# Optimization experiments

Hardware: AMD Instinct MI355X
Metric: run time of the kernel (lower is better)

## Reference

```python
import jax, jax.numpy as jnp
import numpy as np

B, S, D = 1, 2048, 1024          # batch, seq, hidden_size
E, K, F = 8, 2, 1408             # n_routed_experts, top_k, moe_intermediate_size
NS = 2                           # n_shared_experts
SCALE = 2.5                      # routed_scaling_factor (norm_topk_prob=True)


def setup_inputs() -> dict:
    key = jax.random.key(0)
    ks = jax.random.split(key, 8)
    s = 0.02
    return {
        "hidden_states": jax.random.normal(ks[0], (B, S, D), jnp.float32),
        "gate_w": jax.random.normal(ks[1], (E, D), jnp.float32) * s,
        "w_gate": jax.random.normal(ks[2], (E, D, F), jnp.float32) * s,
        "w_up": jax.random.normal(ks[3], (E, D, F), jnp.float32) * s,
        "w_down": jax.random.normal(ks[4], (E, F, D), jnp.float32) * s,
        "sw_gate": jax.random.normal(ks[5], (D, F * NS), jnp.float32) * s,
        "sw_up": jax.random.normal(ks[6], (D, F * NS), jnp.float32) * s,
        "sw_down": jax.random.normal(ks[7], (F * NS, D), jnp.float32) * s,
    }


def _swiglu_mlp(x, wg, wu, wd):
    # down( silu(gate(x)) * up(x) )
    return (jax.nn.silu(x @ wg) * (x @ wu)) @ wd


def reference(hidden_states, gate_w, w_gate, w_up, w_down, sw_gate, sw_up, sw_down):
    identity = hidden_states
    x = hidden_states.reshape(-1, hidden_states.shape[-1])  # [T, D]
    T = x.shape[0]

    # --- MoEGate (softmax scoring, greedy top-k, normalized + scaled) ---
    logits = x.astype(jnp.float32) @ gate_w.astype(jnp.float32).T  # [T, E]
    scores = jax.nn.softmax(logits, axis=-1)
    topk_w, topk_i = jax.lax.top_k(scores, K)                      # [T, K]
    topk_w = topk_w / (topk_w.sum(-1, keepdims=True) + 1e-20) * SCALE

    # Dense combine weights [T, E]: topk weight where routed, 0 elsewhere.
    combine = jnp.zeros((T, E), jnp.float32).at[
        jnp.arange(T)[:, None], topk_i
    ].set(topk_w)

    # --- Routed experts as grouped GEMMs (same math as sort/dispatch loop) ---
    g = jax.nn.silu(jnp.einsum('td,edf->etf', x, w_gate)) \
        * jnp.einsum('td,edf->etf', x, w_up)                       # [E, T, F]
    expert_out = jnp.einsum('etf,efd->etd', g, w_down)             # [E, T, D]
    y = jnp.einsum('te,etd->td', combine, expert_out).astype(x.dtype)
    y = y.reshape(identity.shape)

    # --- Shared expert ---
    return y + _swiglu_mlp(identity, sw_gate, sw_up, sw_down)
```

## Files before the change

kernel.cpp:

```cpp
#include <hip/hip_runtime.h>
#include <hip/hip_bf16.h>
#include <stdint.h>

#define TT 2048
#define DD 1024
#define NE 8
#define FR 1408
#define FS 2816
#define RSCALE 2.5f
#define NSLOT (TT * 2)
#define TSH 4096

typedef __attribute__((ext_vector_type(8))) short bf16x8;
typedef __attribute__((ext_vector_type(4))) float f32x4;

__device__ __forceinline__ short f2bf(float f) {
  uint32_t u = __builtin_bit_cast(uint32_t, f);
  u = (u + 0x7fffu + ((u >> 16) & 1u)) >> 16;
  return (short)(uint16_t)u;
}

__global__ void cast_kernel(const float* __restrict__ in, short* __restrict__ out, int n) {
  int i = (blockIdx.x * blockDim.x + threadIdx.x) * 4;
  if (i >= n) return;
  float4 v = *(const float4*)(in + i);
  short4 o;
  o.x = f2bf(v.x); o.y = f2bf(v.y); o.z = f2bf(v.z); o.w = f2bf(v.w);
  *(short4*)(out + i) = o;
}

__global__ void __launch_bounds__(256) tcastV(const float* __restrict__ in0,
                                              const float* __restrict__ in1,
                                              short* __restrict__ out0, short* __restrict__ out1,
                                              int K, int N, int64_t zin, int64_t zout, int nz) {
  int z = blockIdx.z;
  const float* in;
  short* out;
  if (z < nz) { in = in0 + (int64_t)z * zin; out = out0 + (int64_t)z * zout; }
  else        { int zz = z - nz; in = in1 + (int64_t)zz * zin; out = out1 + (int64_t)zz * zout; }
  __shared__ float tile[32][33];
  const int k0 = blockIdx.y * 32, n0 = blockIdx.x * 32;
  const int tid = threadIdx.x;
  const int lr = tid >> 5, lc = tid & 31;
#pragma unroll
  for (int i = 0; i < 4; ++i)
    tile[lr + i * 8][lc] = in[(int64_t)(k0 + lr + i * 8) * N + n0 + lc];
  __syncthreads();
  const int nl = tid >> 3, kq = (tid & 7) * 4;
  short4 o;
  o.x = f2bf(tile[kq + 0][nl]); o.y = f2bf(tile[kq + 1][nl]);
  o.z = f2bf(tile[kq + 2][nl]); o.w = f2bf(tile[kq + 3][nl]);
  *(short4*)&out[(int64_t)(n0 + nl) * K + k0 + kq] = o;
}

__global__ void gate_kernel(const float* __restrict__ x, const float* __restrict__ gw,
                            int* __restrict__ te, float* __restrict__ tw) {
  int t = blockIdx.x;
  int lane = threadIdx.x;
  const float* xr = x + (size_t)t * DD + lane * 16;
  float4 xv[4];
#pragma unroll
  for (int i = 0; i < 4; ++i) xv[i] = *(const float4*)(xr + i * 4);
  float p[NE];
#pragma unroll
  for (int e = 0; e < NE; ++e) {
    const float* gr = gw + (size_t)e * DD + lane * 16;
    float s = 0.f;
#pragma unroll
    for (int i = 0; i < 4; ++i) {
      float4 g = *(const float4*)(gr + i * 4);
      s += xv[i].x * g.x + xv[i].y * g.y + xv[i].z * g.z + xv[i].w * g.w;
    }
    p[e] = s;
  }
#pragma unroll
  for (int off = 32; off >= 1; off >>= 1) {
#pragma unroll
    for (int e = 0; e < NE; ++e) p[e] += __shfl_xor(p[e], off);
  }
  float mx = p[0];
#pragma unroll
  for (int e = 1; e < NE; ++e) mx = fmaxf(mx, p[e]);
  float s = 0.f, sc[NE];
#pragma unroll
  for (int e = 0; e < NE; ++e) { sc[e] = expf(p[e] - mx); s += sc[e]; }
  float inv = 1.f / s;
#pragma unroll
  for (int e = 0; e < NE; ++e) sc[e] *= inv;
  int e1 = 0;
#pragma unroll
  for (int e = 1; e < NE; ++e) if (sc[e] > sc[e1]) e1 = e;
  int e2 = (e1 == 0) ? 1 : 0;
#pragma unroll
  for (int e = 0; e < NE; ++e) if (e != e1 && sc[e] > sc[e2]) e2 = e;
  float w1 = sc[e1], w2 = sc[e2];
  float k = RSCALE / (w1 + w2 + 1e-20f);
  if (lane == 0) {
    te[t * 2] = e1;     tw[t * 2] = w1 * k;
    te[t * 2 + 1] = e2; tw[t * 2 + 1] = w2 * k;
  }
}

__global__ void __launch_bounds__(1024) scatter_kernel(const int* __restrict__ te,
                                                       const float* __restrict__ tw,
                                                       int* __restrict__ cnt, int* __restrict__ off,
                                                       int* __restrict__ eidx, float* __restrict__ wslot) {
  __shared__ int lcnt[NE], loff[NE], lrun[NE];
  const int tid = threadIdx.x;
  if (tid < NE) lcnt[tid] = 0;
  __syncthreads();
  for (int s = tid; s < NSLOT; s += 1024) atomicAdd(&lcnt[te[s]], 1);
  __syncthreads();
  if (tid == 0) {
    int acc = 0;
    for (int e = 0; e < NE; ++e) { loff[e] = acc; lrun[e] = acc; acc += lcnt[e]; }
  }
  __syncthreads();
  for (int s = tid; s < NSLOT; s += 1024) {
    int e = te[s];
    int p = atomicAdd(&lrun[e], 1);
    eidx[p] = s >> 1;
    wslot[p] = tw[s];
  }
  if (tid < NE) { cnt[tid] = lcnt[tid]; off[tid] = loff[tid]; }
}

__device__ __forceinline__ void stage32(const short* __restrict__ g, int64_t ld,
                                        short* l, int wave, int lane) {
#pragma unroll
  for (int i = 0; i < 2; ++i) {
    int c = i * 256 + wave * 64 + lane;
    __builtin_amdgcn_global_load_lds(
        (const __attribute__((address_space(1))) void*)(g + (int64_t)(c >> 2) * ld + (c & 3) * 8),
        (__attribute__((address_space(3))) void*)(l + (i * 256 + wave * 64) * 8),
        16, 0, 0);
  }
}

template <int MODE>
__global__ void __launch_bounds__(256) moe_gemm(
    const short* __restrict__ Ab, int lda,
    const short* __restrict__ B0b, const short* __restrict__ B1b, int ldb,
    int K,
    short* __restrict__ Hb, int ldh,
    float* __restrict__ Ob) {
  const int brow = blockIdx.y * 128;
  const int bcol = blockIdx.x * 128;

  __shared__ __align__(16) short lA[2 * TSH];
  __shared__ __align__(16) short lB0[2 * TSH];
  __shared__ __align__(16) short lB1[(MODE == 0) ? 2 * TSH : 8];

  const int tid = threadIdx.x;
  const int lane = tid & 63;
  const int wave = tid >> 6;
  const int wr = wave >> 1, wc = wave & 1;

  f32x4 acc0[4][4];
  f32x4 acc1[(MODE == 0) ? 4 : 1][(MODE == 0) ? 4 : 1];
#pragma unroll
  for (int m = 0; m < 4; ++m)
#pragma unroll
    for (int n = 0; n < 4; ++n) {
      acc0[m][n] = (f32x4){0.f, 0.f, 0.f, 0.f};
      if constexpr (MODE == 0) acc1[m][n] = (f32x4){0.f, 0.f, 0.f, 0.f};
    }

  const short* Abase = Ab + (int64_t)brow * lda;
  const short* B0base = B0b + (int64_t)bcol * ldb;
  const short* B1base = (MODE == 0) ? (B1b + (int64_t)bcol * ldb) : nullptr;

  auto STAGE = [&](int buf, int k0) {
    stage32(Abase + k0, lda, lA + buf * TSH, wave, lane);
    stage32(B0base + k0, ldb, lB0 + buf * TSH, wave, lane);
    if constexpr (MODE == 0) stage32(B1base + k0, ldb, lB1 + buf * TSH, wave, lane);
  };

  STAGE(0, 0);
  __syncthreads();
  int cur = 0;
  for (int k0 = 0; k0 < K; k0 += 32) {
    if (k0 + 32 < K) STAGE(cur ^ 1, k0 + 32);
    const short* A_ = lA + cur * TSH;
    const short* B0_ = lB0 + cur * TSH;
    const short* B1_ = lB1 + cur * TSH;
#pragma unroll
    for (int m = 0; m < 4; ++m) {
      bf16x8 af = *(const bf16x8*)&A_[(wr * 64 + m * 16 + (lane & 15)) * 32 + (lane >> 4) * 8];
#pragma unroll
      for (int n = 0; n < 4; ++n) {
        bf16x8 b0 = *(const bf16x8*)&B0_[(wc * 64 + n * 16 + (lane & 15)) * 32 + (lane >> 4) * 8];
        acc0[m][n] = __builtin_amdgcn_mfma_f32_16x16x32_bf16(af, b0, acc0[m][n], 0, 0, 0);
        if constexpr (MODE == 0) {
          bf16x8 b1 = *(const bf16x8*)&B1_[(wc * 64 + n * 16 + (lane & 15)) * 32 + (lane >> 4) * 8];
          acc1[m][n] = __builtin_amdgcn_mfma_f32_16x16x32_bf16(af, b1, acc1[m][n], 0, 0, 0);
        }
      }
    }
    __syncthreads();
    cur ^= 1;
  }

#pragma unroll
  for (int m = 0; m < 4; ++m)
#pragma unroll
    for (int n = 0; n < 4; ++n)
#pragma unroll
      for (int r = 0; r < 4; ++r) {
        int row = brow + wr * 64 + m * 16 + (lane >> 4) * 4 + r;
        int col = bcol + wc * 64 + n * 16 + (lane & 15);
        float g = acc0[m][n][r];
        if constexpr (MODE == 0) {
          float u = acc1[m][n][r];
          Hb[(int64_t)row * ldh + col] = f2bf(g / (1.f + __expf(-g)) * u);
        } else {
          Ob[(int64_t)row * DD + col] = g;
        }
      }
}

__global__ void __launch_bounds__(256) gu_sparse(
    const short* __restrict__ Xb,
    const short* __restrict__ wgT, const short* __restrict__ wuT,
    short* __restrict__ Hr,
    const int* __restrict__ cnt, const int* __restrict__ off,
    const int* __restrict__ eidx) {
  const int z = blockIdx.z;
  const int c = cnt[z];
  const int m0 = blockIdx.y * 128;
  if (m0 >= c) return;
  const int base = off[z];
  const int bcol = blockIdx.x * 128;

  __shared__ __align__(16) short lA[2 * TSH];
  __shared__ __align__(16) short lB0[2 * TSH];
  __shared__ __align__(16) short lB1[2 * TSH];

  const int tid = threadIdx.x;
  const int lane = tid & 63;
  const int wave = tid >> 6;
  const int wr = wave >> 1, wc = wave & 1;

  const short* aptr[2];
#pragma unroll
  for (int i = 0; i < 2; ++i) {
    int cl = i * 256 + wave * 64 + lane;
    int r = cl >> 2;
    int sv = m0 + r; if (sv >= c) sv = c - 1;
    aptr[i] = Xb + (int64_t)eidx[base + sv] * DD + (cl & 3) * 8;
  }

  f32x4 acc0[4][4], acc1[4][4];
#pragma unroll
  for (int m = 0; m < 4; ++m)
#pragma unroll
    for (int n = 0; n < 4; ++n) {
      acc0[m][n] = (f32x4){0.f, 0.f, 0.f, 0.f};
      acc1[m][n] = (f32x4){0.f, 0.f, 0.f, 0.f};
    }

  const short* B0base = wgT + (int64_t)z * FR * DD + (int64_t)bcol * DD;
  const short* B1base = wuT + (int64_t)z * FR * DD + (int64_t)bcol * DD;

  auto STAGE = [&](int buf, int k0) {
#pragma unroll
    for (int i = 0; i < 2; ++i)
      __builtin_amdgcn_global_load_lds(
          (const __attribute__((address_space(1))) void*)(aptr[i] + k0),
          (__attribute__((address_space(3))) void*)(lA + buf * TSH + (i * 256 + wave * 64) * 8),
          16, 0, 0);
    stage32(B0base + k0, DD, lB0 + buf * TSH, wave, lane);
    stage32(B1base + k0, DD, lB1 + buf * TSH, wave, lane);
  };

  STAGE(0, 0);
  __syncthreads();
  int cur = 0;
  for (int k0 = 0; k0 < DD; k0 += 32) {
    if (k0 + 32 < DD) STAGE(cur ^ 1, k0 + 32);
    const short* A_ = lA + cur * TSH;
    const short* B0_ = lB0 + cur * TSH;
    const short* B1_ = lB1 + cur * TSH;
#pragma unroll
    for (int m = 0; m < 4; ++m) {
      bf16x8 af = *(const bf16x8*)&A_[(wr * 64 + m * 16 + (lane & 15)) * 32 + (lane >> 4) * 8];
#pragma unroll
      for (int n = 0; n < 4; ++n) {
        bf16x8 b0 = *(const bf16x8*)&B0_[(wc * 64 + n * 16 + (lane & 15)) * 32 + (lane >> 4) * 8];
        acc0[m][n] = __builtin_amdgcn_mfma_f32_16x16x32_bf16(af, b0, acc0[m][n], 0, 0, 0);
        bf16x8 b1 = *(const bf16x8*)&B1_[(wc * 64 + n * 16 + (lane & 15)) * 32 + (lane >> 4) * 8];
        acc1[m][n] = __builtin_amdgcn_mfma_f32_16x16x32_bf16(af, b1, acc1[m][n], 0, 0, 0);
      }
    }
    __syncthreads();
    cur ^= 1;
  }

#pragma unroll
  for (int m = 0; m < 4; ++m)
#pragma unroll
    for (int n = 0; n < 4; ++n)
#pragma unroll
      for (int r = 0; r < 4; ++r) {
        int rl = wr * 64 + m * 16 + (lane >> 4) * 4 + r;
        int sv = m0 + rl;
        if (sv < c) {
          int col = bcol + wc * 64 + n * 16 + (lane & 15);
          float g = acc0[m][n][r], u = acc1[m][n][r];
          Hr[(int64_t)(base + sv) * FR + col] = f2bf(g / (1.f + __expf(-g)) * u);
        }
      }
}

__global__ void __launch_bounds__(256) down_sparse(
    const short* __restrict__ Hr,
    const short* __restrict__ wdT,
    float* __restrict__ out,
    const int* __restrict__ cnt, const int* __restrict__ off,
    const int* __restrict__ eidx, const float* __restrict__ wslot) {
  const int z = blockIdx.z;
  const int c = cnt[z];
  const int m0 = blockIdx.y * 128;
  if (m0 >= c) return;
  const int base = off[z];
  const int bcol = blockIdx.x * 128;

  __shared__ __align__(16) short lA[2 * TSH];
  __shared__ __align__(16) short lB0[2 * TSH];
  __shared__ int lTok[128];
  __shared__ float lW[128];

  const int tid = threadIdx.x;
  const int lane = tid & 63;
  const int wave = tid >> 6;
  const int wr = wave >> 1, wc = wave & 1;

  if (tid < 128) {
    int sv = m0 + tid;
    if (sv < c) { lTok[tid] = eidx[base + sv]; lW[tid] = wslot[base + sv]; }
    else lW[tid] = 0.f;
  }

  f32x4 acc0[4][4];
#pragma unroll
  for (int m = 0; m < 4; ++m)
#pragma unroll
    for (int n = 0; n < 4; ++n) acc0[m][n] = (f32x4){0.f, 0.f, 0.f, 0.f};

  const short* B0base = wdT + (int64_t)z * DD * FR + (int64_t)bcol * FR;

  auto STAGE = [&](int buf, int k0) {
#pragma unroll
    for (int i = 0; i < 2; ++i) {
      int cl = i * 256 + wave * 64 + lane;
      int r = cl >> 2;
      int sv = m0 + r; if (sv >= c) sv = c - 1;
      __builtin_amdgcn_global_load_lds(
          (const __attribute__((address_space(1))) void*)(Hr + (int64_t)(base + sv) * FR + k0 + (cl & 3) * 8),
          (__attribute__((address_space(3))) void*)(lA + buf * TSH + (i * 256 + wave * 64) * 8),
          16, 0, 0);
    }
    stage32(B0base + k0, FR, lB0 + buf * TSH, wave, lane);
  };

  STAGE(0, 0);
  __syncthreads();
  int cur = 0;
  for (int k0 = 0; k0 < FR; k0 += 32) {
    if (k0 + 32 < FR) STAGE(cur ^ 1, k0 + 32);
    const short* A_ = lA + cur * TSH;
    const short* B0_ = lB0 + cur * TSH;
#pragma unroll
    for (int m = 0; m < 4; ++m) {
      bf16x8 af = *(const bf16x8*)&A_[(wr * 64 + m * 16 + (lane & 15)) * 32 + (lane >> 4) * 8];
#pragma unroll
      for (int n = 0; n < 4; ++n) {
        bf16x8 b0 = *(const bf16x8*)&B0_[(wc * 64 + n * 16 + (lane & 15)) * 32 + (lane >> 4) * 8];
        acc0[m][n] = __builtin_amdgcn_mfma_f32_16x16x32_bf16(af, b0, acc0[m][n], 0, 0, 0);
      }
    }
    __syncthreads();
    cur ^= 1;
  }

#pragma unroll
  for (int m = 0; m < 4; ++m)
#pragma unroll
    for (int n = 0; n < 4; ++n)
#pragma unroll
      for (int r = 0; r < 4; ++r) {
        int rl = wr * 64 + m * 16 + (lane >> 4) * 4 + r;
        if (m0 + rl < c) {
          int col = bcol + wc * 64 + n * 16 + (lane & 15);
          atomicAdd(&out[(int64_t)lTok[rl] * DD + col], lW[rl] * acc0[m][n][r]);
        }
      }
}

extern "C" void kernel_launch(void* const* d_in, const int* in_sizes, int n_in,
                              void* d_out, int out_size, void* d_ws, size_t ws_size,
                              hipStream_t stream) {
  const float* x       = (const float*)d_in[0];
  const float* gw      = (const float*)d_in[1];
  const float* w_gate  = (const float*)d_in[2];
  const float* w_up    = (const float*)d_in[3];
  const float* w_down  = (const float*)d_in[4];
  const float* sw_gate = (const float*)d_in[5];
  const float* sw_up   = (const float*)d_in[6];
  const float* sw_down = (const float*)d_in[7];
  float* out = (float*)d_out;

  char* ws = (char*)d_ws;
  int*   te    = (int*)ws;    ws += NSLOT * 4;
  float* tw    = (float*)ws;  ws += NSLOT * 4;
  int*   cnt   = (int*)ws;    ws += 64 * 4;
  int*   off   = (int*)ws;    ws += 64 * 4;
  int*   eidx  = (int*)ws;    ws += NSLOT * 4;
  float* wslot = (float*)ws;  ws += NSLOT * 4;
  ws = (char*)(((uintptr_t)ws + 255) & ~(uintptr_t)255);
  short* Xb   = (short*)ws;  ws += (size_t)TT * DD * 2;
  short* Hs   = (short*)ws;  ws += (size_t)TT * FS * 2;
  short* Hr   = (short*)ws;  ws += (size_t)NSLOT * FR * 2;
  short* wgT  = (short*)ws;  ws += (size_t)NE * FR * DD * 2;
  short* wuT  = (short*)ws;  ws += (size_t)NE * FR * DD * 2;
  short* wdT  = (short*)ws;  ws += (size_t)NE * DD * FR * 2;
  short* swgT = (short*)ws;  ws += (size_t)FS * DD * 2;
  short* swuT = (short*)ws;  ws += (size_t)FS * DD * 2;
  short* swdT = (short*)ws;

  cast_kernel<<<dim3((TT * DD) / 1024), dim3(256), 0, stream>>>(x, Xb, TT * DD);
  gate_kernel<<<dim3(TT), dim3(64), 0, stream>>>(x, gw, te, tw);
  scatter_kernel<<<dim3(1), dim3(1024), 0, stream>>>(te, tw, cnt, off, eidx, wslot);
  tcastV<<<dim3(FR / 32, DD / 32, 2 * NE), dim3(256), 0, stream>>>(
      w_gate, w_up, wgT, wuT, DD, FR, (int64_t)DD * FR, (int64_t)FR * DD, NE);
  tcastV<<<dim3(DD / 32, FR / 32, NE), dim3(256), 0, stream>>>(
      w_down, w_down, wdT, wdT, FR, DD, (int64_t)FR * DD, (int64_t)DD * FR, NE);
  tcastV<<<dim3(FS / 32, DD / 32, 2), dim3(256), 0, stream>>>(
      sw_gate, sw_up, swgT, swuT, DD, FS, 0, 0, 1);
  tcastV<<<dim3(DD / 32, FS / 32, 1), dim3(256), 0, stream>>>(
      sw_down, sw_down, swdT, swdT, FS, DD, 0, 0, 1);
  moe_gemm<0><<<dim3(FS / 128, TT / 128), dim3(256), 0, stream>>>(
      Xb, DD, swgT, swuT, DD, DD, Hs, FS, nullptr);
  gu_sparse<<<dim3(FR / 128, TT / 128, NE), dim3(256), 0, stream>>>(
      Xb, wgT, wuT, Hr, cnt, off, eidx);
  moe_gemm<1><<<dim3(DD / 128, TT / 128), dim3(256), 0, stream>>>(
      Hs, FS, swdT, nullptr, FS, FS, nullptr, 0, out);
  down_sparse<<<dim3(DD / 128, TT / 128, NE), dim3(256), 0, stream>>>(
      Hr, wdT, out, cnt, off, eidx, wslot);
}
```

Baseline: 480.4 us.

## Fold shared expert into grouped routed GEMMs as two virtual experts

The shared expert's gate/up and down GEMMs become two extra virtual experts, each with identity token lists and weight 1, inside the sparse grouped kernels. This cuts the launch count from four GEMM launches to two, so shared and routed work share one grid and can fill the GPU together. In exchange, out must be zeroed with a memset and all contributions accumulate via the atomic/scatter path. The grid y dimension also grows to NSLOT/128, so many blocks exit early.

```diff
diff --git a/kernel.cpp b/kernel.cpp
--- a/kernel.cpp
+++ b/kernel.cpp
@@ -9,6 +9,8 @@
 #define FS 2816
 #define RSCALE 2.5f
 #define NSLOT (TT * 2)
+#define NVSLOT (NSLOT + 2 * TT)
+#define NZ (NE + 2)
 #define TSH 4096
 
 typedef __attribute__((ext_vector_type(8))) short bf16x8;
@@ -122,7 +124,13 @@
     eidx[p] = s >> 1;
     wslot[p] = tw[s];
   }
+  for (int t = tid; t < TT; t += 1024) {
+    eidx[NSLOT + t] = t;       wslot[NSLOT + t] = 1.0f;
+    eidx[NSLOT + TT + t] = t;  wslot[NSLOT + TT + t] = 1.0f;
+  }
   if (tid < NE) { cnt[tid] = lcnt[tid]; off[tid] = loff[tid]; }
+  if (tid == NE)     { cnt[NE] = TT;     off[NE] = NSLOT; }
+  if (tid == NE + 1) { cnt[NE + 1] = TT; off[NE + 1] = NSLOT + TT; }
 }
 
 __device__ __forceinline__ void stage32(const short* __restrict__ g, int64_t ld,
@@ -137,92 +145,11 @@
   }
 }
 
-template <int MODE>
-__global__ void __launch_bounds__(256) moe_gemm(
-    const short* __restrict__ Ab, int lda,
-    const short* __restrict__ B0b, const short* __restrict__ B1b, int ldb,
-    int K,
-    short* __restrict__ Hb, int ldh,
-    float* __restrict__ Ob) {
-  const int brow = blockIdx.y * 128;
-  const int bcol = blockIdx.x * 128;
-
-  __shared__ __align__(16) short lA[2 * TSH];
-  __shared__ __align__(16) short lB0[2 * TSH];
-  __shared__ __align__(16) short lB1[(MODE == 0) ? 2 * TSH : 8];
-
-  const int tid = threadIdx.x;
-  const int lane = tid & 63;
-  const int wave = tid >> 6;
-  const int wr = wave >> 1, wc = wave & 1;
-
-  f32x4 acc0[4][4];
-  f32x4 acc1[(MODE == 0) ? 4 : 1][(MODE == 0) ? 4 : 1];
-#pragma unroll
-  for (int m = 0; m < 4; ++m)
-#pragma unroll
-    for (int n = 0; n < 4; ++n) {
-      acc0[m][n] = (f32x4){0.f, 0.f, 0.f, 0.f};
-      if constexpr (MODE == 0) acc1[m][n] = (f32x4){0.f, 0.f, 0.f, 0.f};
-    }
-
-  const short* Abase = Ab + (int64_t)brow * lda;
-  const short* B0base = B0b + (int64_t)bcol * ldb;
-  const short* B1base = (MODE == 0) ? (B1b + (int64_t)bcol * ldb) : nullptr;
-
-  auto STAGE = [&](int buf, int k0) {
-    stage32(Abase + k0, lda, lA + buf * TSH, wave, lane);
-    stage32(B0base + k0, ldb, lB0 + buf * TSH, wave, lane);
-    if constexpr (MODE == 0) stage32(B1base + k0, ldb, lB1 + buf * TSH, wave, lane);
-  };
-
-  STAGE(0, 0);
-  __syncthreads();
-  int cur = 0;
-  for (int k0 = 0; k0 < K; k0 += 32) {
-    if (k0 + 32 < K) STAGE(cur ^ 1, k0 + 32);
-    const short* A_ = lA + cur * TSH;
-    const short* B0_ = lB0 + cur * TSH;
-    const short* B1_ = lB1 + cur * TSH;
-#pragma unroll
-    for (int m = 0; m < 4; ++m) {
-      bf16x8 af = *(const bf16x8*)&A_[(wr * 64 + m * 16 + (lane & 15)) * 32 + (lane >> 4) * 8];
-#pragma unroll
-      for (int n = 0; n < 4; ++n) {
-        bf16x8 b0 = *(const bf16x8*)&B0_[(wc * 64 + n * 16 + (lane & 15)) * 32 + (lane >> 4) * 8];
-        acc0[m][n] = __builtin_amdgcn_mfma_f32_16x16x32_bf16(af, b0, acc0[m][n], 0, 0, 0);
-        if constexpr (MODE == 0) {
-          bf16x8 b1 = *(const bf16x8*)&B1_[(wc * 64 + n * 16 + (lane & 15)) * 32 + (lane >> 4) * 8];
-          acc1[m][n] = __builtin_amdgcn_mfma_f32_16x16x32_bf16(af, b1, acc1[m][n], 0, 0, 0);
-        }
-      }
-    }
-    __syncthreads();
-    cur ^= 1;
-  }
-
-#pragma unroll
-  for (int m = 0; m < 4; ++m)
-#pragma unroll
-    for (int n = 0; n < 4; ++n)
-#pragma unroll
-      for (int r = 0; r < 4; ++r) {
-        int row = brow + wr * 64 + m * 16 + (lane >> 4) * 4 + r;
-        int col = bcol + wc * 64 + n * 16 + (lane & 15);
-        float g = acc0[m][n][r];
-        if constexpr (MODE == 0) {
-          float u = acc1[m][n][r];
-          Hb[(int64_t)row * ldh + col] = f2bf(g / (1.f + __expf(-g)) * u);
-        } else {
-          Ob[(int64_t)row * DD + col] = g;
-        }
-      }
-}
-
-__global__ void __launch_bounds__(256) gu_sparse(
+__global__ void __launch_bounds__(256) gu_all(
     const short* __restrict__ Xb,
     const short* __restrict__ wgT, const short* __restrict__ wuT,
-    short* __restrict__ Hr,
+    const short* __restrict__ swgT, const short* __restrict__ swuT,
+    short* __restrict__ Hall,
     const int* __restrict__ cnt, const int* __restrict__ off,
     const int* __restrict__ eidx) {
   const int z = blockIdx.z;
@@ -241,6 +168,16 @@
   const int wave = tid >> 6;
   const int wr = wave >> 1, wc = wave & 1;
 
+  const short *B0base, *B1base;
+  if (z < NE) {
+    B0base = wgT + ((int64_t)z * FR + bcol) * DD;
+    B1base = wuT + ((int64_t)z * FR + bcol) * DD;
+  } else {
+    int h = z - NE;
+    B0base = swgT + ((int64_t)h * FR + bcol) * DD;
+    B1base = swuT + ((int64_t)h * FR + bcol) * DD;
+  }
+
   const short* aptr[2];
 #pragma unroll
   for (int i = 0; i < 2; ++i) {
@@ -258,9 +195,6 @@
       acc0[m][n] = (f32x4){0.f, 0.f, 0.f, 0.f};
       acc1[m][n] = (f32x4){0.f, 0.f, 0.f, 0.f};
     }
-
-  const short* B0base = wgT + (int64_t)z * FR * DD + (int64_t)bcol * DD;
-  const short* B1base = wuT + (int64_t)z * FR * DD + (int64_t)bcol * DD;
 
   auto STAGE = [&](int buf, int k0) {
 #pragma unroll
@@ -307,14 +241,14 @@
         if (sv < c) {
           int col = bcol + wc * 64 + n * 16 + (lane & 15);
           float g = acc0[m][n][r], u = acc1[m][n][r];
-          Hr[(int64_t)(base + sv) * FR + col] = f2bf(g / (1.f + __expf(-g)) * u);
+          Hall[(int64_t)(base + sv) * FR + col] = f2bf(g / (1.f + __expf(-g)) * u);
         }
       }
 }
 
-__global__ void __launch_bounds__(256) down_sparse(
-    const short* __restrict__ Hr,
-    const short* __restrict__ wdT,
+__global__ void __launch_bounds__(256) down_all(
+    const short* __restrict__ Hall,
+    const short* __restrict__ wdT, const short* __restrict__ swdT,
     float* __restrict__ out,
     const int* __restrict__ cnt, const int* __restrict__ off,
     const int* __restrict__ eidx, const float* __restrict__ wslot) {
@@ -335,6 +269,11 @@
   const int wave = tid >> 6;
   const int wr = wave >> 1, wc = wave & 1;
 
+  const short* B0base;
+  int64_t ldb;
+  if (z < NE) { B0base = wdT + ((int64_t)z * DD + bcol) * FR; ldb = FR; }
+  else        { B0base = swdT + (int64_t)bcol * FS + (int64_t)(z - NE) * FR; ldb = FS; }
+
   if (tid < 128) {
     int sv = m0 + tid;
     if (sv < c) { lTok[tid] = eidx[base + sv]; lW[tid] = wslot[base + sv]; }
@@ -346,8 +285,6 @@
   for (int m = 0; m < 4; ++m)
 #pragma unroll
     for (int n = 0; n < 4; ++n) acc0[m][n] = (f32x4){0.f, 0.f, 0.f, 0.f};
-
-  const short* B0base = wdT + (int64_t)z * DD * FR + (int64_t)bcol * FR;
 
   auto STAGE = [&](int buf, int k0) {
 #pragma unroll
@@ -356,11 +293,11 @@
       int r = cl >> 2;
       int sv = m0 + r; if (sv >= c) sv = c - 1;
       __builtin_amdgcn_global_load_lds(
-          (const __attribute__((address_space(1))) void*)(Hr + (int64_t)(base + sv) * FR + k0 + (cl & 3) * 8),
+          (const __attribute__((address_space(1))) void*)(Hall + (int64_t)(base + sv) * FR + k0 + (cl & 3) * 8),
           (__attribute__((address_space(3))) void*)(lA + buf * TSH + (i * 256 + wave * 64) * 8),
           16, 0, 0);
     }
-    stage32(B0base + k0, FR, lB0 + buf * TSH, wave, lane);
+    stage32(B0base + k0, ldb, lB0 + buf * TSH, wave, lane);
   };
 
   STAGE(0, 0);
@@ -415,12 +352,11 @@
   float* tw    = (float*)ws;  ws += NSLOT * 4;
   int*   cnt   = (int*)ws;    ws += 64 * 4;
   int*   off   = (int*)ws;    ws += 64 * 4;
-  int*   eidx  = (int*)ws;    ws += NSLOT * 4;
-  float* wslot = (float*)ws;  ws += NSLOT * 4;
+  int*   eidx  = (int*)ws;    ws += NVSLOT * 4;
+  float* wslot = (float*)ws;  ws += NVSLOT * 4;
   ws = (char*)(((uintptr_t)ws + 255) & ~(uintptr_t)255);
   short* Xb   = (short*)ws;  ws += (size_t)TT * DD * 2;
-  short* Hs   = (short*)ws;  ws += (size_t)TT * FS * 2;
-  short* Hr   = (short*)ws;  ws += (size_t)NSLOT * FR * 2;
+  short* Hall = (short*)ws;  ws += (size_t)NVSLOT * FR * 2;
   short* wgT  = (short*)ws;  ws += (size_t)NE * FR * DD * 2;
   short* wuT  = (short*)ws;  ws += (size_t)NE * FR * DD * 2;
   short* wdT  = (short*)ws;  ws += (size_t)NE * DD * FR * 2;
@@ -439,12 +375,9 @@
       sw_gate, sw_up, swgT, swuT, DD, FS, 0, 0, 1);
   tcastV<<<dim3(DD / 32, FS / 32, 1), dim3(256), 0, stream>>>(
       sw_down, sw_down, swdT, swdT, FS, DD, 0, 0, 1);
-  moe_gemm<0><<<dim3(FS / 128, TT / 128), dim3(256), 0, stream>>>(
-      Xb, DD, swgT, swuT, DD, DD, Hs, FS, nullptr);
-  gu_sparse<<<dim3(FR / 128, TT / 128, NE), dim3(256), 0, stream>>>(
-      Xb, wgT, wuT, Hr, cnt, off, eidx);
-  moe_gemm<1><<<dim3(DD / 128, TT / 128), dim3(256), 0, stream>>>(
-      Hs, FS, swdT, nullptr, FS, FS, nullptr, 0, out);
-  down_sparse<<<dim3(DD / 128, TT / 128, NE), dim3(256), 0, stream>>>(
-      Hr, wdT, out, cnt, off, eidx, wslot);
-}
+  hipMemsetAsync(out, 0, (size_t)TT * DD * 4, stream);
+  gu_all<<<dim3(FR / 128, NSLOT / 128, NZ), dim3(256), 0, stream>>>(
+      Xb, wgT, wuT, swgT, swuT, Hall, cnt, off, eidx);
+  down_all<<<dim3(DD / 128, NSLOT / 128, NZ), dim3(256), 0, stream>>>(
+      Hall, wdT, swdT, out, cnt, off, eidx, wslot);
+}
```

Measured after the change: 434.4 us. 9.6% less time.
